# Optimization experiments

Measured on AMD Instinct MI355X. Metric: run time of the kernel, lower is better.

## Reference

```python
import jax, jax.numpy as jnp
import numpy as np

N = 10000
IN_DIM = 512
OUT_DIM = 128
E = 262144


def setup_inputs() -> dict:
    key = jax.random.key(0)
    ks = jax.random.split(key, 7)
    x = jax.random.normal(ks[0], (N, IN_DIM), dtype=jnp.float32)
    adj = jax.random.uniform(ks[1], (N, N), dtype=jnp.float32) * (1.0 / N)
    # xavier-ish scaled params
    weight = jax.random.normal(ks[2], (IN_DIM, OUT_DIM), dtype=jnp.float32) * (1.0 / np.sqrt(IN_DIM))
    weight_two = jax.random.normal(ks[3], (2 * OUT_DIM, OUT_DIM), dtype=jnp.float32) * (1.0 / np.sqrt(2 * OUT_DIM))
    weight_three = jax.random.normal(ks[4], (2 * OUT_DIM, 1), dtype=jnp.float32) * (1.0 / np.sqrt(2 * OUT_DIM))
    train_edges = jax.random.randint(ks[5], (E, 2), 0, N, dtype=jnp.int32)
    train_false_edges = jax.random.randint(ks[6], (E, 2), 0, N, dtype=jnp.int32)
    return {
        "x": x,
        "adj": adj,
        "weight": weight,
        "weight_two": weight_two,
        "weight_three": weight_three,
        "train_edges": train_edges,
        "train_false_edges": train_false_edges,
    }


def reference(x, adj, weight, weight_two, weight_three, train_edges, train_false_edges):
    # encode: z = adj @ (x @ W)   -> [N, OUT_DIM]
    z = adj @ (x @ weight)
    # decode: vectorized per-edge gather of both endpoints
    edges = jnp.concatenate([train_edges, train_false_edges], axis=0)  # [2E, 2]
    zi = z[edges[:, 0]]  # [2E, OUT_DIM]
    zj = z[edges[:, 1]]  # [2E, OUT_DIM]
    z_pair = jnp.concatenate([zi, zj], axis=1)          # [2E, 2*OUT_DIM]
    z_mult = zi * zj                                     # [2E, OUT_DIM]
    z_pair = jax.nn.relu(z_pair) @ weight_two            # [2E, OUT_DIM]
    logits = jnp.concatenate([z_pair, z_mult], axis=1) @ weight_three  # [2E, 1]
    return jax.nn.sigmoid(logits)
```

## Files before the change

kernel.cpp:

```cpp
#include <hip/hip_runtime.h>

#define N_NODES 10000
#define IN_DIM  512
#define OUT_DIM 128
#define NE      262144
#define K_DIM   10000
#define HT_S    10112

#define BM 64
#define BN 128
#define BK 128
#define SPLITS 8
#define KSTEPS_TOTAL 79
#define STEPS_PER_SPLIT 10

typedef __attribute__((ext_vector_type(8))) __bf16 bf16x8;
typedef __attribute__((ext_vector_type(4))) float  f32x4;

__device__ inline ushort f2bf(float f) {
    uint u = __float_as_uint(f);
    return (ushort)((u + 0x7fffu + ((u >> 16) & 1u)) >> 16);
}
__device__ inline float bflo(uint u) { return __uint_as_float(u << 16); }
__device__ inline float bfhi(uint u) { return __uint_as_float(u & 0xffff0000u); }

__device__ __forceinline__ void gl2lds16(const void* g, void* l) {
    __builtin_amdgcn_global_load_lds(
        (const __attribute__((address_space(1))) void*)g,
        (__attribute__((address_space(3))) void*)l, 16, 0, 0);
}

__global__ __launch_bounds__(256) void k_prep(const float* __restrict__ w,
                                              const float* __restrict__ w2,
                                              const float* __restrict__ w3,
                                              ushort* __restrict__ WT,
                                              float* __restrict__ v,
                                              ushort* __restrict__ hT) {
    const int t = threadIdx.x;
    for (int idx = blockIdx.x * 256 + t; idx < IN_DIM * OUT_DIM; idx += gridDim.x * 256) {
        int k = idx >> 7, n = idx & 127;
        WT[n * IN_DIM + k] = f2bf(w[idx]);
    }
    if (blockIdx.x == 0) {
        float s = 0.f;
        for (int j = 0; j < OUT_DIM; ++j) s += w2[t * OUT_DIM + j] * w3[j];
        v[t] = s;
    }
    if (blockIdx.x == 1) {
        for (int idx = t; idx < 128 * (HT_S - N_NODES); idx += 256) {
            int c = idx / (HT_S - N_NODES), r = idx % (HT_S - N_NODES);
            hT[(size_t)c * HT_S + N_NODES + r] = 0;
        }
    }
}

__global__ __launch_bounds__(256) void k_xw(const float* __restrict__ x,
                                            const ushort* __restrict__ WT,
                                            ushort* __restrict__ hT) {
    const int tid = threadIdx.x, wave = tid >> 6, lane = tid & 63;
    const int lr = lane & 15, lg = lane >> 4;
    const int r0 = blockIdx.x * 16;
    const int c0 = wave * 32;
    const float* pA = x + (size_t)(r0 + lr) * IN_DIM;

    f32x4 acc[2];
#pragma unroll
    for (int nf = 0; nf < 2; ++nf) acc[nf] = (f32x4){0.f, 0.f, 0.f, 0.f};

#pragma unroll
    for (int st = 0; st < 8; ++st) {
        const int k0 = st * 64;
        bf16x8 abf[2];
#pragma unroll
        for (int kh = 0; kh < 2; ++kh) {
            float4 a0 = *(const float4*)(pA + k0 + kh * 32 + lg * 8);
            float4 a1 = *(const float4*)(pA + k0 + kh * 32 + lg * 8 + 4);
            ushort* ap = (ushort*)&abf[kh];
            ap[0] = f2bf(a0.x); ap[1] = f2bf(a0.y); ap[2] = f2bf(a0.z); ap[3] = f2bf(a0.w);
            ap[4] = f2bf(a1.x); ap[5] = f2bf(a1.y); ap[6] = f2bf(a1.z); ap[7] = f2bf(a1.w);
        }
#pragma unroll
        for (int kh = 0; kh < 2; ++kh)
#pragma unroll
            for (int nf = 0; nf < 2; ++nf) {
                bf16x8 bfv = *(const bf16x8*)(WT + (size_t)(c0 + nf * 16 + lr) * IN_DIM + k0 + kh * 32 + lg * 8);
                acc[nf] = __builtin_amdgcn_mfma_f32_16x16x32_bf16(abf[kh], bfv, acc[nf], 0, 0, 0);
            }
    }

    const int m0 = r0 + lg * 4;
#pragma unroll
    for (int nf = 0; nf < 2; ++nf) {
        int c = c0 + nf * 16 + lr;
        ushort4 pk;
        pk.x = f2bf(acc[nf][0]); pk.y = f2bf(acc[nf][1]);
        pk.z = f2bf(acc[nf][2]); pk.w = f2bf(acc[nf][3]);
        *(ushort4*)(hT + (size_t)c * HT_S + m0) = pk;
    }
}

__global__ __launch_bounds__(256) void k_adj(const float* __restrict__ adj,
                                             const ushort* __restrict__ hT,
                                             float* __restrict__ zp) {
    __shared__ ushort Bs[BN * BK];

    const int tid = threadIdx.x, wave = tid >> 6, lane = tid & 63;
    const int lr = lane & 15, lg = lane >> 4;
    const int m0 = blockIdx.x * BM;
    const int split = blockIdx.y;
    const int step0 = split * STEPS_PER_SPLIT;
    const int step1 = min(step0 + STEPS_PER_SPLIT, KSTEPS_TOTAL);

    long  bbase[8];
    char* bldst[8];
#pragma unroll
    for (int q = 0; q < 8; ++q) {
        int c = tid + q * 256;
        int row = c >> 4, ch = c & 15;
        bbase[q] = (long)row * HT_S + (long)((ch ^ (row & 15)) * 8);
        bldst[q] = (char*)Bs + c * 16;
    }

    const int arow = min(m0 + wave * 16 + lr, N_NODES - 1);
    const float* pA = adj + (size_t)arow * K_DIM;

    f32x4 acc[8];
#pragma unroll
    for (int nf = 0; nf < 8; ++nf) acc[nf] = (f32x4){0.f, 0.f, 0.f, 0.f};

    const char* Bb = (const char*)Bs;

    for (int st = step0; st < step1; ++st) {
        const int k0 = st * BK;

#pragma unroll
        for (int q = 0; q < 8; ++q)
            gl2lds16(hT + (bbase[q] + k0), bldst[q]);

        float4 fa[4][2];
#pragma unroll
        for (int kh = 0; kh < 4; ++kh) {
            int kk = k0 + kh * 32 + lg * 8;
            int kc = (kk <= K_DIM - 8) ? kk : (K_DIM - 8);
            fa[kh][0] = *(const float4*)(pA + kc);
            fa[kh][1] = *(const float4*)(pA + kc + 4);
        }

        __syncthreads();

#pragma unroll
        for (int kh = 0; kh < 4; ++kh) {
            bf16x8 abf;
            ushort* ap = (ushort*)&abf;
            const float* f0 = (const float*)&fa[kh][0];
#pragma unroll
            for (int e = 0; e < 8; ++e) ap[e] = f2bf(f0[e]);
#pragma unroll
            for (int nf = 0; nf < 8; ++nf) {
                int brow = nf * 16 + lr;
                bf16x8 bv = *(const bf16x8*)(Bb + brow * 256 + (((kh * 4 + lg) ^ (brow & 15)) * 16));
                acc[nf] = __builtin_amdgcn_mfma_f32_16x16x32_bf16(abf, bv, acc[nf], 0, 0, 0);
            }
        }

        __syncthreads();
    }

    float* out = zp + (size_t)split * N_NODES * OUT_DIM;
    const int orow = m0 + wave * 16 + lg * 4;
#pragma unroll
    for (int nf = 0; nf < 8; ++nf)
#pragma unroll
        for (int r = 0; r < 4; ++r) {
            int row = orow + r;
            if (row < N_NODES)
                out[(size_t)row * OUT_DIM + nf * 16 + lr] = acc[nf][r];
        }
}

__global__ __launch_bounds__(256) void k_node(const float* __restrict__ zp,
                                              const float* __restrict__ v,
                                              float* __restrict__ a,
                                              float* __restrict__ b,
                                              ushort* __restrict__ zb) {
    const int wave = threadIdx.x >> 6, lane = threadIdx.x & 63;
    const int i = blockIdx.x * 4 + wave;
    if (i >= N_NODES) return;
    const int k0 = lane, k1 = lane + 64;

    float z0 = 0.f, z1 = 0.f;
#pragma unroll
    for (int s = 0; s < SPLITS; ++s) {
        const float* row = zp + ((size_t)s * N_NODES + i) * OUT_DIM;
        z0 += row[k0];
        z1 += row[k1];
    }
    zb[(size_t)i * OUT_DIM + k0] = f2bf(z0);
    zb[(size_t)i * OUT_DIM + k1] = f2bf(z1);

    float ra = fmaxf(z0, 0.f) * v[k0] + fmaxf(z1, 0.f) * v[k1];
    float rb = fmaxf(z0, 0.f) * v[OUT_DIM + k0] + fmaxf(z1, 0.f) * v[OUT_DIM + k1];
#pragma unroll
    for (int off = 32; off; off >>= 1) {
        ra += __shfl_down(ra, off);
        rb += __shfl_down(rb, off);
    }
    if (lane == 0) { a[i] = ra; b[i] = rb; }
}

__global__ __launch_bounds__(256) void k_edge(const int* __restrict__ e_true,
                                              const int* __restrict__ e_false,
                                              const float* __restrict__ a,
                                              const float* __restrict__ b,
                                              const ushort* __restrict__ zb,
                                              const float* __restrict__ w3,
                                              float* __restrict__ out) {
    const int lane = threadIdx.x & 63;
    const int grp  = lane >> 4;
    const int l16  = lane & 15;
    const int gw   = (blockIdx.x * blockDim.x + threadIdx.x) >> 6;
    const int nw   = (gridDim.x * blockDim.x) >> 6;

    const float4 wv0 = *(const float4*)(w3 + OUT_DIM + l16 * 8);
    const float4 wv1 = *(const float4*)(w3 + OUT_DIM + l16 * 8 + 4);

    for (int e4 = gw; e4 < (2 * NE) / 4; e4 += nw) {
        const int e = e4 * 4 + grp;
        int2 ij = (e < NE) ? ((const int2*)e_true)[e] : ((const int2*)e_false)[e - NE];
        const int i = ij.x, j = ij.y;

        uint4 zi = *(const uint4*)(zb + (size_t)i * OUT_DIM + l16 * 8);
        uint4 zj = *(const uint4*)(zb + (size_t)j * OUT_DIM + l16 * 8);

        float d;
        d  = wv0.x * bflo(zi.x) * bflo(zj.x);
        d += wv0.y * bfhi(zi.x) * bfhi(zj.x);
        d += wv0.z * bflo(zi.y) * bflo(zj.y);
        d += wv0.w * bfhi(zi.y) * bfhi(zj.y);
        d += wv1.x * bflo(zi.z) * bflo(zj.z);
        d += wv1.y * bfhi(zi.z) * bfhi(zj.z);
        d += wv1.z * bflo(zi.w) * bflo(zj.w);
        d += wv1.w * bfhi(zi.w) * bfhi(zj.w);

#pragma unroll
        for (int off = 8; off; off >>= 1) d += __shfl_xor(d, off, 64);
        if (l16 == 0) {
            float logit = a[i] + b[j] + d;
            out[e] = 1.0f / (1.0f + __expf(-logit));
        }
    }
}

extern "C" void kernel_launch(void* const* d_in, const int* in_sizes, int n_in,
                              void* d_out, int out_size, void* d_ws, size_t ws_size,
                              hipStream_t stream) {
    const float* x      = (const float*)d_in[0];
    const float* adj    = (const float*)d_in[1];
    const float* w      = (const float*)d_in[2];
    const float* w2     = (const float*)d_in[3];
    const float* w3     = (const float*)d_in[4];
    const int* e_true   = (const int*)d_in[5];
    const int* e_false  = (const int*)d_in[6];
    float* out          = (float*)d_out;

    char* ws = (char*)d_ws;
    ushort* hT  = (ushort*)(ws);
    float*  zp  = (float*)(ws + 2588672);
    float*  v   = (float*)(ws + 43548672);
    float*  a   = (float*)(ws + 43549696);
    float*  b   = (float*)(ws + 43589696);
    ushort* zb  = (ushort*)(ws + 43629696);
    ushort* WT  = (ushort*)(ws + 46189696);

    k_prep<<<64, 256, 0, stream>>>(w, w2, w3, WT, v, hT);
    k_xw<<<625, 256, 0, stream>>>(x, WT, hT);
    k_adj<<<dim3(157, SPLITS), 256, 0, stream>>>(adj, hT, zp);
    k_node<<<2500, 256, 0, stream>>>(zp, v, a, b, zb);
    k_edge<<<2048, 256, 0, stream>>>(e_true, e_false, a, b, zb, w3, out);
}
```

Baseline: 187.9 us.

## Fuse split-K reduction and node epilogue into adj GEMM via last-block counter

Removes the separate k_node kernel. Each adj GEMM tile now bumps an atomic per-row-tile counter after writing its partial sums, and the last split to arrive reduces all partials for that 64-row tile, writing bf16 z and the per-node a/b projections. This saves one kernel launch and lets the reduction overlap with other tiles' GEMM work. In exchange it adds a memset, atomics and fences, and leaves the reduction to a single block per tile, so the tail can be serialized.

After: 348.1 us. +85.2%, slower.

```diff
diff --git a/kernel.cpp b/kernel.cpp
--- a/kernel.cpp
+++ b/kernel.cpp
@@ -101,7 +101,12 @@
 
 __global__ __launch_bounds__(256) void k_adj(const float* __restrict__ adj,
                                              const ushort* __restrict__ hT,
-                                             float* __restrict__ zp) {
+                                             float* __restrict__ zp,
+                                             const float* __restrict__ v,
+                                             float* __restrict__ a,
+                                             float* __restrict__ b,
+                                             ushort* __restrict__ zb,
+                                             uint* __restrict__ tilecnt) {
     __shared__ ushort Bs[BN * BK];
 
     const int tid = threadIdx.x, wave = tid >> 6, lane = tid & 63;
@@ -166,7 +171,7 @@
         __syncthreads();
     }
 
-    float* out = zp + (size_t)split * N_NODES * OUT_DIM;
+    float* outp = zp + (size_t)split * N_NODES * OUT_DIM;
     const int orow = m0 + wave * 16 + lg * 4;
 #pragma unroll
     for (int nf = 0; nf < 8; ++nf)
@@ -174,38 +179,42 @@
         for (int r = 0; r < 4; ++r) {
             int row = orow + r;
             if (row < N_NODES)
-                out[(size_t)row * OUT_DIM + nf * 16 + lr] = acc[nf][r];
-        }
-}
-
-__global__ __launch_bounds__(256) void k_node(const float* __restrict__ zp,
-                                              const float* __restrict__ v,
-                                              float* __restrict__ a,
-                                              float* __restrict__ b,
-                                              ushort* __restrict__ zb) {
-    const int wave = threadIdx.x >> 6, lane = threadIdx.x & 63;
-    const int i = blockIdx.x * 4 + wave;
-    if (i >= N_NODES) return;
-    const int k0 = lane, k1 = lane + 64;
-
-    float z0 = 0.f, z1 = 0.f;
-#pragma unroll
-    for (int s = 0; s < SPLITS; ++s) {
-        const float* row = zp + ((size_t)s * N_NODES + i) * OUT_DIM;
-        z0 += row[k0];
-        z1 += row[k1];
-    }
-    zb[(size_t)i * OUT_DIM + k0] = f2bf(z0);
-    zb[(size_t)i * OUT_DIM + k1] = f2bf(z1);
-
-    float ra = fmaxf(z0, 0.f) * v[k0] + fmaxf(z1, 0.f) * v[k1];
-    float rb = fmaxf(z0, 0.f) * v[OUT_DIM + k0] + fmaxf(z1, 0.f) * v[OUT_DIM + k1];
-#pragma unroll
-    for (int off = 32; off; off >>= 1) {
-        ra += __shfl_down(ra, off);
-        rb += __shfl_down(rb, off);
-    }
-    if (lane == 0) { a[i] = ra; b[i] = rb; }
+                outp[(size_t)row * OUT_DIM + nf * 16 + lr] = acc[nf][r];
+        }
+
+    __syncthreads();
+    int* lastFlag = (int*)Bs;
+    if (tid == 0) {
+        uint old = __hip_atomic_fetch_add(&tilecnt[blockIdx.x], 1u,
+                                          __ATOMIC_ACQ_REL, __HIP_MEMORY_SCOPE_AGENT);
+        *lastFlag = (old == SPLITS - 1);
+    }
+    __syncthreads();
+    if (!*lastFlag) return;
+    __threadfence();
+
+    for (int rr = 0; rr < 16; ++rr) {
+        const int i = m0 + wave * 16 + rr;
+        if (i >= N_NODES) continue;
+        float z0 = 0.f, z1 = 0.f;
+#pragma unroll
+        for (int s = 0; s < SPLITS; ++s) {
+            const volatile float* row = zp + ((size_t)s * N_NODES + i) * OUT_DIM;
+            z0 += row[lane];
+            z1 += row[lane + 64];
+        }
+        zb[(size_t)i * OUT_DIM + lane]      = f2bf(z0);
+        zb[(size_t)i * OUT_DIM + lane + 64] = f2bf(z1);
+
+        float ra = fmaxf(z0, 0.f) * v[lane] + fmaxf(z1, 0.f) * v[lane + 64];
+        float rb = fmaxf(z0, 0.f) * v[OUT_DIM + lane] + fmaxf(z1, 0.f) * v[OUT_DIM + lane + 64];
+#pragma unroll
+        for (int off = 32; off; off >>= 1) {
+            ra += __shfl_down(ra, off);
+            rb += __shfl_down(rb, off);
+        }
+        if (lane == 0) { a[i] = ra; b[i] = rb; }
+    }
 }
 
 __global__ __launch_bounds__(256) void k_edge(const int* __restrict__ e_true,
@@ -264,17 +273,18 @@
     float* out          = (float*)d_out;
 
     char* ws = (char*)d_ws;
-    ushort* hT  = (ushort*)(ws);
-    float*  zp  = (float*)(ws + 2588672);
-    float*  v   = (float*)(ws + 43548672);
-    float*  a   = (float*)(ws + 43549696);
-    float*  b   = (float*)(ws + 43589696);
-    ushort* zb  = (ushort*)(ws + 43629696);
-    ushort* WT  = (ushort*)(ws + 46189696);
-
+    ushort* hT      = (ushort*)(ws);
+    float*  zp      = (float*)(ws + 2588672);
+    float*  v       = (float*)(ws + 43548672);
+    float*  a       = (float*)(ws + 43549696);
+    float*  b       = (float*)(ws + 43589696);
+    ushort* zb      = (ushort*)(ws + 43629696);
+    ushort* WT      = (ushort*)(ws + 46189696);
+    uint*   tilecnt = (uint*)(ws + 46320768);
+
+    hipMemsetAsync(tilecnt, 0, 1024, stream);
     k_prep<<<64, 256, 0, stream>>>(w, w2, w3, WT, v, hT);
     k_xw<<<625, 256, 0, stream>>>(x, WT, hT);
-    k_adj<<<dim3(157, SPLITS), 256, 0, stream>>>(adj, hT, zp);
-    k_node<<<2500, 256, 0, stream>>>(zp, v, a, b, zb);
+    k_adj<<<dim3(157, SPLITS), 256, 0, stream>>>(adj, hT, zp, v, a, b, zb, tilecnt);
     k_edge<<<2048, 256, 0, stream>>>(e_true, e_false, a, b, zb, w3, out);
 }
```
